# Kernel optimization log

Measured on AMD Instinct MI355X. Metric: run time of the kernel, lower is better.

## Reference

```python
import jax, jax.numpy as jnp
import numpy as np


def setup_inputs() -> dict:
    key = jax.random.key(0)
    ka, kb = jax.random.split(key)
    B, S, I, J = 8, 8192, 256, 256
    a = jax.random.normal(ka, (B, S, I), dtype=jnp.float32)
    b = jax.random.normal(kb, (B, S, J), dtype=jnp.float32)
    return {"a": a, "b": b}


def reference(a, b):
    # mean_s(a_si outer b_sj) == (a^T @ b) / s, without materializing [*, i, j, s]
    s = a.shape[-2]
    out = jnp.einsum('...si,...sj->...ij', a, b) / s  # [*, i, j]
    return out
```

## Files before the change

### kernel.cpp

```cpp
#include <hip/hip_runtime.h>

typedef __bf16 bf16x8 __attribute__((ext_vector_type(8)));
typedef float f32x16 __attribute__((ext_vector_type(16)));
typedef float f32x4 __attribute__((ext_vector_type(4)));

#define S_TOTAL 8192
#define DIM 256
#define BK 16
#define SPLIT 32

__global__ __launch_bounds__(512, 4) void opm_partial(
    const float* __restrict__ A, const float* __restrict__ Bm,
    __bf16* __restrict__ dstbf, float* __restrict__ dstf32,
    int split, int kc, float scale)
{
    __shared__ float lA[3][BK * 256];
    __shared__ float lB[3][BK * 128];

    const int tid = threadIdx.x;
    const int w   = tid >> 6;
    const int l   = tid & 63;

    const int bid = blockIdx.x;
    const int x  = bid & 7;
    const int k  = bid >> 3;
    const int jh = k & 1;
    const int p  = (k >> 1) * 8 + x;
    const int batch = p / split;
    const int sp    = p % split;

    const long long base = (long long)batch * S_TOTAL * DIM;
    const int s0 = sp * kc;
    const int wr = w >> 1, wc = w & 1;
    const int lane31 = l & 31;
    const int hi = l >> 5;
    const int niter = kc / BK;

    f32x16 acc[2][2] = {};

    auto issue = [&](int it) {
        const int b3 = it % 3;
        const long long sb = (long long)(s0 + it * BK);
        __builtin_amdgcn_global_load_lds(
            (const __attribute__((address_space(1))) unsigned int*)(A + base + (sb + w) * DIM + 4 * l),
            (__attribute__((address_space(3))) unsigned int*)&lA[b3][w * 256], 16, 0, 0);
        __builtin_amdgcn_global_load_lds(
            (const __attribute__((address_space(1))) unsigned int*)(A + base + (sb + w + 8) * DIM + 4 * l),
            (__attribute__((address_space(3))) unsigned int*)&lA[b3][(w + 8) * 256], 16, 0, 0);
        __builtin_amdgcn_global_load_lds(
            (const __attribute__((address_space(1))) unsigned int*)(Bm + base + (sb + 2 * w + (l >> 5)) * DIM + jh * 128 + 4 * (l & 31)),
            (__attribute__((address_space(3))) unsigned int*)&lB[b3][2 * w * 128], 16, 0, 0);
    };

    auto compute = [&](int b3) {
        const int i0 = wr * 64 + lane31;
        const int j0 = wc * 64 + lane31;
        bf16x8 af[2], bfv[2];
        #pragma unroll
        for (int mi = 0; mi < 2; ++mi)
            #pragma unroll
            for (int e = 0; e < 8; ++e)
                af[mi][e] = (__bf16)lA[b3][(hi * 8 + e) * 256 + i0 + mi * 32];
        #pragma unroll
        for (int nj = 0; nj < 2; ++nj)
            #pragma unroll
            for (int e = 0; e < 8; ++e)
                bfv[nj][e] = (__bf16)lB[b3][(hi * 8 + e) * 128 + j0 + nj * 32];
        #pragma unroll
        for (int mi = 0; mi < 2; ++mi)
            #pragma unroll
            for (int nj = 0; nj < 2; ++nj)
                acc[mi][nj] = __builtin_amdgcn_mfma_f32_32x32x16_bf16(
                    af[mi], bfv[nj], acc[mi][nj], 0, 0, 0);
    };

    issue(0);
    issue(1);

    for (int it = 0; it < niter; ++it) {
        if (it + 1 < niter) asm volatile("s_waitcnt vmcnt(3)" ::: "memory");
        else                asm volatile("s_waitcnt vmcnt(0)" ::: "memory");
        __builtin_amdgcn_s_barrier();
        if (it + 2 < niter) issue(it + 2);
        compute(it % 3);
    }

    if (dstf32) {
        float* o = dstf32 + (long long)batch * (256 * 256) + jh * 128;
        #pragma unroll
        for (int mi = 0; mi < 2; ++mi)
        #pragma unroll
        for (int nj = 0; nj < 2; ++nj)
        #pragma unroll
        for (int q = 0; q < 16; ++q) {
            const int row = (q & 3) + 8 * (q >> 2) + 4 * hi;
            const int i = wr * 64 + mi * 32 + row;
            const int j = wc * 64 + nj * 32 + lane31;
            o[i * 256 + j] = acc[mi][nj][q] * scale;
        }
    } else {
        __bf16* o = dstbf + (long long)(batch * split + sp) * (256 * 256) + jh * 128;
        __bf16* ebuf = (__bf16*)&lA[0][0];
        #pragma unroll
        for (int band = 0; band < 4; ++band) {
            __syncthreads();
            if (wr == band) {
                #pragma unroll
                for (int mi = 0; mi < 2; ++mi)
                #pragma unroll
                for (int nj = 0; nj < 2; ++nj)
                #pragma unroll
                for (int q = 0; q < 16; ++q) {
                    const int row = mi * 32 + (q & 3) + 8 * (q >> 2) + 4 * hi;
                    const int col = wc * 64 + nj * 32 + lane31;
                    ebuf[row * 128 + col] = (__bf16)(acc[mi][nj][q] * scale);
                }
            }
            __syncthreads();
            #pragma unroll
            for (int h = 0; h < 2; ++h) {
                const int G = tid + h * 512;
                const int r = G >> 4, c8 = (G & 15) * 8;
                bf16x8 v = *(const bf16x8*)&ebuf[r * 128 + c8];
                *(bf16x8*)&o[(band * 64 + r) * 256 + c8] = v;
            }
        }
    }
}

__global__ __launch_bounds__(256) void opm_reduce32(
    const __bf16* __restrict__ ws, float* __restrict__ out)
{
    const int idx = blockIdx.x * 256 + threadIdx.x;
    const int b = idx >> 13;
    const int r = idx & 8191;
    const bf16x8* p = (const bf16x8*)ws + ((long long)b * SPLIT) * 8192 + r;

    bf16x8 v[SPLIT];
    #pragma unroll
    for (int sp = 0; sp < SPLIT; ++sp) v[sp] = p[sp * 8192];

    float s[8] = {0.f, 0.f, 0.f, 0.f, 0.f, 0.f, 0.f, 0.f};
    #pragma unroll
    for (int sp = 0; sp < SPLIT; ++sp)
        #pragma unroll
        for (int e = 0; e < 8; ++e) s[e] += (float)v[sp][e];

    f32x4 lo = { s[0], s[1], s[2], s[3] };
    f32x4 hiv = { s[4], s[5], s[6], s[7] };
    lo  *= (1.0f / 8192.0f);
    hiv *= (1.0f / 8192.0f);
    ((f32x4*)out)[idx * 2]     = lo;
    ((f32x4*)out)[idx * 2 + 1] = hiv;
}

extern "C" void kernel_launch(void* const* d_in, const int* in_sizes, int n_in,
                              void* d_out, int out_size, void* d_ws, size_t ws_size,
                              hipStream_t stream)
{
    (void)in_sizes; (void)n_in; (void)out_size;
    const float* A  = (const float*)d_in[0];
    const float* Bm = (const float*)d_in[1];
    float* out = (float*)d_out;

    if (ws_size >= (size_t)8 * SPLIT * 65536 * sizeof(__bf16)) {
        opm_partial<<<16 * SPLIT, 512, 0, stream>>>(A, Bm, (__bf16*)d_ws, nullptr,
                                                    SPLIT, S_TOTAL / SPLIT, 1.0f);
        opm_reduce32<<<256, 256, 0, stream>>>((const __bf16*)d_ws, out);
    } else {
        opm_partial<<<16, 512, 0, stream>>>(A, Bm, nullptr, out, 1, S_TOTAL, 1.0f / 8192.0f);
    }
}
```

Measured before the change: 39.02 us.

## Split output columns into quarters and halve S-split count

Result: slower. 41.53 us (+6.4%).

```diff
diff --git a/kernel.cpp b/kernel.cpp
--- a/kernel.cpp
+++ b/kernel.cpp
@@ -7,27 +7,28 @@
 #define S_TOTAL 8192
 #define DIM 256
 #define BK 16
-#define SPLIT 32
+#define NSP 16
 
 __global__ __launch_bounds__(512, 4) void opm_partial(
     const float* __restrict__ A, const float* __restrict__ Bm,
     __bf16* __restrict__ dstbf, float* __restrict__ dstf32,
-    int split, int kc, float scale)
+    int nsp, int kc, float scale)
 {
     __shared__ float lA[3][BK * 256];
-    __shared__ float lB[3][BK * 128];
+    __shared__ float lB[3][BK * 64];
 
     const int tid = threadIdx.x;
     const int w   = tid >> 6;
     const int l   = tid & 63;
 
     const int bid = blockIdx.x;
-    const int x  = bid & 7;
-    const int k  = bid >> 3;
-    const int jh = k & 1;
-    const int p  = (k >> 1) * 8 + x;
-    const int batch = p / split;
-    const int sp    = p % split;
+    const int x   = bid & 7;
+    const int s   = bid >> 3;
+    const int jq  = s & 3;
+    const int gx  = s >> 2;
+    const int g   = gx * 8 + x;
+    const int batch = g / nsp;
+    const int sp    = g % nsp;
 
     const long long base = (long long)batch * S_TOTAL * DIM;
     const int s0 = sp * kc;
@@ -36,7 +37,7 @@
     const int hi = l >> 5;
     const int niter = kc / BK;
 
-    f32x16 acc[2][2] = {};
+    f32x16 acc[2] = {};
 
     auto issue = [&](int it) {
         const int b3 = it % 3;
@@ -47,107 +48,106 @@
         __builtin_amdgcn_global_load_lds(
             (const __attribute__((address_space(1))) unsigned int*)(A + base + (sb + w + 8) * DIM + 4 * l),
             (__attribute__((address_space(3))) unsigned int*)&lA[b3][(w + 8) * 256], 16, 0, 0);
-        __builtin_amdgcn_global_load_lds(
-            (const __attribute__((address_space(1))) unsigned int*)(Bm + base + (sb + 2 * w + (l >> 5)) * DIM + jh * 128 + 4 * (l & 31)),
-            (__attribute__((address_space(3))) unsigned int*)&lB[b3][2 * w * 128], 16, 0, 0);
+        if (w < 4) {
+            __builtin_amdgcn_global_load_lds(
+                (const __attribute__((address_space(1))) unsigned int*)(Bm + base + (sb + 4 * w + (l >> 4)) * DIM + jq * 64 + 4 * (l & 15)),
+                (__attribute__((address_space(3))) unsigned int*)&lB[b3][4 * w * 64], 16, 0, 0);
+        }
     };
 
     auto compute = [&](int b3) {
         const int i0 = wr * 64 + lane31;
-        const int j0 = wc * 64 + lane31;
-        bf16x8 af[2], bfv[2];
+        const int j0 = wc * 32 + lane31;
+        bf16x8 af[2], bfv;
         #pragma unroll
         for (int mi = 0; mi < 2; ++mi)
             #pragma unroll
             for (int e = 0; e < 8; ++e)
                 af[mi][e] = (__bf16)lA[b3][(hi * 8 + e) * 256 + i0 + mi * 32];
         #pragma unroll
-        for (int nj = 0; nj < 2; ++nj)
-            #pragma unroll
-            for (int e = 0; e < 8; ++e)
-                bfv[nj][e] = (__bf16)lB[b3][(hi * 8 + e) * 128 + j0 + nj * 32];
-        #pragma unroll
-        for (int mi = 0; mi < 2; ++mi)
-            #pragma unroll
-            for (int nj = 0; nj < 2; ++nj)
-                acc[mi][nj] = __builtin_amdgcn_mfma_f32_32x32x16_bf16(
-                    af[mi], bfv[nj], acc[mi][nj], 0, 0, 0);
+        for (int e = 0; e < 8; ++e)
+            bfv[e] = (__bf16)lB[b3][(hi * 8 + e) * 64 + j0];
+        acc[0] = __builtin_amdgcn_mfma_f32_32x32x16_bf16(af[0], bfv, acc[0], 0, 0, 0);
+        acc[1] = __builtin_amdgcn_mfma_f32_32x32x16_bf16(af[1], bfv, acc[1], 0, 0, 0);
     };
 
     issue(0);
     issue(1);
 
     for (int it = 0; it < niter; ++it) {
-        if (it + 1 < niter) asm volatile("s_waitcnt vmcnt(3)" ::: "memory");
-        else                asm volatile("s_waitcnt vmcnt(0)" ::: "memory");
+        const int rem = niter - 1 - it;
+        if (w < 4) {
+            if (rem >= 1) asm volatile("s_waitcnt vmcnt(3)" ::: "memory");
+            else          asm volatile("s_waitcnt vmcnt(0)" ::: "memory");
+        } else {
+            if (rem >= 1) asm volatile("s_waitcnt vmcnt(2)" ::: "memory");
+            else          asm volatile("s_waitcnt vmcnt(0)" ::: "memory");
+        }
         __builtin_amdgcn_s_barrier();
         if (it + 2 < niter) issue(it + 2);
         compute(it % 3);
     }
 
     if (dstf32) {
-        float* o = dstf32 + (long long)batch * (256 * 256) + jh * 128;
+        float* o = dstf32 + (long long)batch * (256 * 256) + jq * 64;
         #pragma unroll
         for (int mi = 0; mi < 2; ++mi)
-        #pragma unroll
-        for (int nj = 0; nj < 2; ++nj)
         #pragma unroll
         for (int q = 0; q < 16; ++q) {
             const int row = (q & 3) + 8 * (q >> 2) + 4 * hi;
             const int i = wr * 64 + mi * 32 + row;
-            const int j = wc * 64 + nj * 32 + lane31;
-            o[i * 256 + j] = acc[mi][nj][q] * scale;
+            const int j = wc * 32 + lane31;
+            o[i * 256 + j] = acc[mi][q] * scale;
         }
     } else {
-        __bf16* o = dstbf + (long long)(batch * split + sp) * (256 * 256) + jh * 128;
+        __bf16* o = dstbf + (long long)((batch * nsp + sp) * 4 + jq) * 16384;
         __bf16* ebuf = (__bf16*)&lA[0][0];
         #pragma unroll
-        for (int band = 0; band < 4; ++band) {
+        for (int band = 0; band < 2; ++band) {
             __syncthreads();
-            if (wr == band) {
+            if ((wr >> 1) == band) {
                 #pragma unroll
                 for (int mi = 0; mi < 2; ++mi)
                 #pragma unroll
-                for (int nj = 0; nj < 2; ++nj)
-                #pragma unroll
                 for (int q = 0; q < 16; ++q) {
-                    const int row = mi * 32 + (q & 3) + 8 * (q >> 2) + 4 * hi;
-                    const int col = wc * 64 + nj * 32 + lane31;
-                    ebuf[row * 128 + col] = (__bf16)(acc[mi][nj][q] * scale);
+                    const int lr = (wr & 1) * 64 + mi * 32 + (q & 3) + 8 * (q >> 2) + 4 * hi;
+                    ebuf[lr * 64 + wc * 32 + lane31] = (__bf16)(acc[mi][q] * scale);
                 }
             }
             __syncthreads();
             #pragma unroll
             for (int h = 0; h < 2; ++h) {
                 const int G = tid + h * 512;
-                const int r = G >> 4, c8 = (G & 15) * 8;
-                bf16x8 v = *(const bf16x8*)&ebuf[r * 128 + c8];
-                *(bf16x8*)&o[(band * 64 + r) * 256 + c8] = v;
+                *(bf16x8*)&o[band * 8192 + G * 8] = *(const bf16x8*)&ebuf[G * 8];
             }
         }
     }
 }
 
-__global__ __launch_bounds__(256) void opm_reduce32(
+__global__ __launch_bounds__(256) void opm_reduce16(
     const __bf16* __restrict__ ws, float* __restrict__ out)
 {
     const int idx = blockIdx.x * 256 + threadIdx.x;
-    const int b = idx >> 13;
-    const int r = idx & 8191;
-    const bf16x8* p = (const bf16x8*)ws + ((long long)b * SPLIT) * 8192 + r;
+    const int batch = idx >> 13;
+    const int gg  = idx & 8191;
+    const int i   = gg >> 5;
+    const int jgc = gg & 31;
+    const int jq  = jgc >> 3;
+    const int c8  = (jgc & 7) * 8;
 
-    bf16x8 v[SPLIT];
+    const bf16x8* p = (const bf16x8*)(ws + ((long long)(batch * NSP) * 4 + jq) * 16384 + i * 64 + c8);
+    bf16x8 v[NSP];
     #pragma unroll
-    for (int sp = 0; sp < SPLIT; ++sp) v[sp] = p[sp * 8192];
+    for (int sp = 0; sp < NSP; ++sp) v[sp] = p[sp * 8192];
 
-    float s[8] = {0.f, 0.f, 0.f, 0.f, 0.f, 0.f, 0.f, 0.f};
+    float sacc[8] = {0.f, 0.f, 0.f, 0.f, 0.f, 0.f, 0.f, 0.f};
     #pragma unroll
-    for (int sp = 0; sp < SPLIT; ++sp)
+    for (int sp = 0; sp < NSP; ++sp)
         #pragma unroll
-        for (int e = 0; e < 8; ++e) s[e] += (float)v[sp][e];
+        for (int e = 0; e < 8; ++e) sacc[e] += (float)v[sp][e];
 
-    f32x4 lo = { s[0], s[1], s[2], s[3] };
-    f32x4 hiv = { s[4], s[5], s[6], s[7] };
+    f32x4 lo = { sacc[0], sacc[1], sacc[2], sacc[3] };
+    f32x4 hiv = { sacc[4], sacc[5], sacc[6], sacc[7] };
     lo  *= (1.0f / 8192.0f);
     hiv *= (1.0f / 8192.0f);
     ((f32x4*)out)[idx * 2]     = lo;
@@ -163,11 +163,11 @@
     const float* Bm = (const float*)d_in[1];
     float* out = (float*)d_out;
 
-    if (ws_size >= (size_t)8 * SPLIT * 65536 * sizeof(__bf16)) {
-        opm_partial<<<16 * SPLIT, 512, 0, stream>>>(A, Bm, (__bf16*)d_ws, nullptr,
-                                                    SPLIT, S_TOTAL / SPLIT, 1.0f);
-        opm_reduce32<<<256, 256, 0, stream>>>((const __bf16*)d_ws, out);
+    if (ws_size >= (size_t)8 * NSP * 4 * 16384 * sizeof(__bf16)) {
+        opm_partial<<<32 * NSP, 512, 0, stream>>>(A, Bm, (__bf16*)d_ws, nullptr,
+                                                  NSP, S_TOTAL / NSP, 1.0f);
+        opm_reduce16<<<256, 256, 0, stream>>>((const __bf16*)d_ws, out);
     } else {
-        opm_partial<<<16, 512, 0, stream>>>(A, Bm, nullptr, out, 1, S_TOTAL, 1.0f / 8192.0f);
+        opm_partial<<<32, 512, 0, stream>>>(A, Bm, nullptr, out, 1, S_TOTAL, 1.0f / 8192.0f);
     }
 }
```
